# Kernel optimization log

Hardware: AMD Instinct MI355X
Metric: run time of the kernel (lower is better)

The kernel has to match this reference:

```python
import jax, jax.numpy as jnp
import numpy as np

N = 100000   # nodes
E = 1600000  # edges (avg degree 16)
D = 128      # input feature dim
H = 64       # hidden dim (hard-coded in Sage.__init__)
C = 40       # output classes


def setup_inputs() -> dict:
    key = jax.random.key(0)
    ks = jax.random.split(key, 9)
    s_in = 1.0 / np.sqrt(D)
    s_h = 1.0 / np.sqrt(H)
    return {
        "x": jax.random.normal(ks[0], (N, D), jnp.float32),
        "edge_index": jax.random.randint(ks[1], (2, E), 0, N, dtype=jnp.int64),
        # SAGEConv params: lin_l acts on aggregated neighbors (carries bias),
        # lin_r acts on the root/self features (no bias), per PyG defaults.
        "W1_l": jax.random.uniform(ks[2], (D, H), jnp.float32, -s_in, s_in),
        "W1_r": jax.random.uniform(ks[3], (D, H), jnp.float32, -s_in, s_in),
        "b1": jax.random.uniform(ks[4], (H,), jnp.float32, -s_in, s_in),
        "W2_l": jax.random.uniform(ks[5], (H, C), jnp.float32, -s_h, s_h),
        "W2_r": jax.random.uniform(ks[6], (H, C), jnp.float32, -s_h, s_h),
        "b2": jax.random.uniform(ks[7], (C,), jnp.float32, -s_h, s_h),
    }


def _sage_conv(x, src, dst, W_l, W_r, b):
    # mean-aggregate neighbor features at destination nodes
    msg = x[src]                                             # [E, F] gather
    summed = jax.ops.segment_sum(msg, dst, num_segments=N)   # [N, F]
    deg = jax.ops.segment_sum(jnp.ones((src.shape[0],), x.dtype), dst,
                              num_segments=N)                # [N]
    agg = summed / jnp.maximum(deg, 1.0)[:, None]
    return agg @ W_l + x @ W_r + b


def reference(x, edge_index, W1_l, W1_r, b1, W2_l, W2_r, b2):
    src, dst = edge_index[0], edge_index[1]
    h = _sage_conv(x, src, dst, W1_l, W1_r, b1)
    h = jax.nn.relu(h)
    # F.dropout(training=False) in eval mode -> identity
    out = _sage_conv(h, src, dst, W2_l, W2_r, b2)
    return jax.nn.log_softmax(out, axis=1)
```

## Files before the change

kernel.cpp:

```cpp
#include <hip/hip_runtime.h>

__device__ __forceinline__ float bf2f(unsigned short u) {
  union { unsigned int i; float f; } c; c.i = ((unsigned int)u) << 16; return c.f;
}
__device__ __forceinline__ unsigned short f2bf(float f) {
  union { float f; unsigned int i; } c; c.f = f;
  unsigned int x = c.i;
  return (unsigned short)((x + 0x7fffu + ((x >> 16) & 1u)) >> 16);
}
__device__ __forceinline__ float lo16(unsigned int w) { return bf2f((unsigned short)(w & 0xffffu)); }
__device__ __forceinline__ float hi16(unsigned int w) { return bf2f((unsigned short)(w >> 16)); }

#define DD 128
#define HH 64
#define CC 40
#define NBUCK 256
#define NCHUNK 128
#define MAXNPB 512
#define NQ 4

using bf16x8 = __attribute__((ext_vector_type(8))) short;
using f32x4  = __attribute__((ext_vector_type(4))) float;

__global__ __launch_bounds__(256) void detect(const unsigned int* e32,
                                              const unsigned int* x32, int* flags) {
  __shared__ unsigned int redOr[256];
  __shared__ int redCnt[256];
  int tid = threadIdx.x;
  unsigned int v = 0;
  for (int i = tid; i < 4096; i += 256) v |= e32[2 * i + 1];
  int cnt = 0;
  for (int i = tid; i < 4096; i += 256) {
    unsigned int w = x32[i];
    unsigned int expo = (w >> 7) & 0xffu;
    unsigned short lo = (unsigned short)(w & 0xffffu);
    if (lo == 0 || (expo >= 100u && expo <= 133u)) cnt++;
  }
  redOr[tid] = v; redCnt[tid] = cnt; __syncthreads();
  for (int s = 128; s > 0; s >>= 1) {
    if (tid < s) { redOr[tid] |= redOr[tid + s]; redCnt[tid] += redCnt[tid + s]; }
    __syncthreads();
  }
  if (tid == 0) {
    flags[0] = (redOr[0] == 0u) ? 1 : 0;
    flags[1] = (redCnt[0] < 2048) ? 1 : 0;
  }
}

__global__ __launch_bounds__(256) void hist_k(const int* e32, int E, int N,
                                              const int* flags, int nodesPerB,
                                              int* histG) {
  __shared__ int cnt[NBUCK];
  int tid = threadIdx.x;
  if (tid < NBUCK) cnt[tid] = 0;
  __syncthreads();
  int isI64 = flags[0];
  int chunk = (E + NCHUNK - 1) / NCHUNK;
  int e0 = blockIdx.x * chunk, e1 = min(e0 + chunk, E);
  for (int i = e0 + tid; i < e1; i += 256) {
    int d = isI64 ? e32[2 * (E + i)] : e32[E + i];
    d = min(max(d, 0), N - 1);
    atomicAdd(&cnt[d / nodesPerB], 1);
  }
  __syncthreads();
  if (tid < NBUCK) histG[tid * NCHUNK + blockIdx.x] = cnt[tid];
}

__global__ void hscan_prepw(const int* histG, int* ohist, int* bbase, int* row_ptr4,
                            int N, int E,
                            const void* W1l, const void* W1r, const void* b1,
                            const void* W2l, const void* W2r, const void* b2,
                            const int* flags, unsigned short* Wb1, unsigned short* Wb2,
                            float* b1f, float* b2f) {
  int tid = threadIdx.x;
  if (blockIdx.x == 1) {
    int isf = flags[1];
    auto rd = [&](const void* p, int i) -> float {
      return isf ? ((const float*)p)[i] : bf2f(((const unsigned short*)p)[i]);
    };
    for (int idx = tid; idx < 128 * 128; idx += 1024) {
      int n = idx >> 7, k = idx & 127;
      float v = (n < HH) ? rd(W1l, k * HH + n) : rd(W1r, k * HH + (n - HH));
      Wb1[idx] = f2bf(v);
    }
    for (int idx = tid; idx < 48 * 128; idx += 1024) {
      int n = idx >> 7, k = idx & 127;
      float v = 0.f;
      if (n < CC) v = (k < HH) ? rd(W2l, k * CC + n) : rd(W2r, (k - HH) * CC + n);
      Wb2[idx] = f2bf(v);
    }
    if (tid < HH) b1f[tid] = rd(b1, tid);
    if (tid < CC) b2f[tid] = rd(b2, tid);
    return;
  }
  __shared__ int tmp[1024];
  int v[32];
  int base = tid * 32;
  int s = 0;
#pragma unroll
  for (int k = 0; k < 32; k++) { v[k] = histG[base + k]; s += v[k]; }
  tmp[tid] = s; __syncthreads();
  for (int st = 1; st < 1024; st <<= 1) {
    int t = (tid >= st) ? tmp[tid - st] : 0;
    __syncthreads();
    tmp[tid] += t;
    __syncthreads();
  }
  int run = tmp[tid] - s;
#pragma unroll
  for (int k = 0; k < 32; k++) { ohist[base + k] = run; run += v[k]; }
  __syncthreads();
  if (tid < NBUCK) bbase[tid] = ohist[tid * NCHUNK];
  if (tid == 0) { bbase[NBUCK] = E; row_ptr4[NQ * N] = E; }
}

__global__ __launch_bounds__(256) void scatter_k(const int* e32, int E, int N,
                                                 const int* flags, int nodesPerB,
                                                 const int* ohist, uint2* ebuf) {
  __shared__ int cur[NBUCK];
  int tid = threadIdx.x;
  if (tid < NBUCK) cur[tid] = ohist[tid * NCHUNK + blockIdx.x];
  __syncthreads();
  int isI64 = flags[0];
  int chunk = (E + NCHUNK - 1) / NCHUNK;
  int e0 = blockIdx.x * chunk, e1 = min(e0 + chunk, E);
  for (int i = e0 + tid; i < e1; i += 256) {
    int s, d;
    if (isI64) { s = e32[2 * i]; d = e32[2 * (E + i)]; }
    else       { s = e32[i];     d = e32[E + i]; }
    s = min(max(s, 0), N - 1);
    d = min(max(d, 0), N - 1);
    int p = atomicAdd(&cur[d / nodesPerB], 1);
    ebuf[p] = make_uint2((unsigned)s, (unsigned)d);
  }
}

__global__ __launch_bounds__(256) void bktB_or_t1(
    const uint2* ebuf, const int* bbase,
    int nbuck, int nodesPerB, int qshift, int* row_ptr4, float* invd, int* col, int N,
    const void* xraw, const int* flags, const unsigned short* Wb1, const float* b1f,
    unsigned short* t1, unsigned short* s1, int T1B) {
  __shared__ int ldsb[MAXNPB * NQ + 256];
  int b = blockIdx.x;
  int tid = threadIdx.x;

  if (b < nbuck) {
    int* cnt = ldsb;
    int* sA  = ldsb + MAXNPB * NQ;
    int base_node = b * nodesPerB;
    int nn = min(nodesPerB, N - base_node);
    if (nn <= 0) return;
    int nk = nn * NQ;
    int eb0 = bbase[b], eb1 = bbase[b + 1];
    int nE = eb1 - eb0;
    const uint2* ee = ebuf + eb0;
    for (int i = tid; i < nk; i += 256) cnt[i] = 0;
    __syncthreads();
    for (int i = tid; i < nE; i += 256) {
      uint2 eg = ee[i];
      int key = ((int)eg.y - base_node) * NQ + (int)(eg.x >> qshift);
      atomicAdd(&cnt[key], 1);
    }
    __syncthreads();
    for (int i = tid; i < nn; i += 256) {
      int d = cnt[NQ * i] + cnt[NQ * i + 1] + cnt[NQ * i + 2] + cnt[NQ * i + 3];
      invd[base_node + i] = 1.0f / (float)max(d, 1);
    }
    __syncthreads();
    int per = (nk + 255) / 256;
    int myb = tid * per;
    int dreg[8];
    int ssum = 0;
#pragma unroll
    for (int k = 0; k < 8; k++) {
      int idx = myb + k;
      int v = (k < per && idx < nk) ? cnt[idx] : 0;
      dreg[k] = v; ssum += v;
    }
    sA[tid] = ssum;
    __syncthreads();
    for (int st = 1; st < 256; st <<= 1) {
      int t = (tid >= st) ? sA[tid - st] : 0;
      __syncthreads();
      sA[tid] += t;
      __syncthreads();
    }
    int run = eb0 + sA[tid] - ssum;
    __syncthreads();
#pragma unroll
    for (int k = 0; k < 8; k++) {
      int idx = myb + k;
      if (k < per && idx < nk) {
        row_ptr4[(size_t)(base_node + (idx >> 2)) * NQ + (idx & 3)] = run;
        cnt[idx] = run;
        run += dreg[k];
      }
    }
    __syncthreads();
    for (int i = tid; i < nE; i += 256) {
      uint2 eg = ee[i];
      int key = ((int)eg.y - base_node) * NQ + (int)(eg.x >> qshift);
      int p = atomicAdd(&cnt[key], 1);
      col[p] = (int)eg.x;
    }
    return;
  }

  int t = b - nbuck;
  if (t >= T1B) return;
  int lane = tid & 63, wv = tid >> 6;
  int nb = t * 64 + wv * 16;
  int oc = lane & 15, kgrp = lane >> 4;
  int node = min(nb + oc, N - 1);
  f32x4 acc[8];
#pragma unroll
  for (int i = 0; i < 8; i++) acc[i] = (f32x4){0.f, 0.f, 0.f, 0.f};

  if (flags[1]) {
    const float4* x4 = (const float4*)xraw;
#pragma unroll
    for (int kb = 0; kb < 4; kb++) {
      int k0 = kb * 32 + kgrp * 8;
      float4 a0 = x4[(size_t)node * 32 + (k0 >> 2)];
      float4 a1 = x4[(size_t)node * 32 + (k0 >> 2) + 1];
      bf16x8 af;
      af[0] = (short)f2bf(a0.x); af[1] = (short)f2bf(a0.y);
      af[2] = (short)f2bf(a0.z); af[3] = (short)f2bf(a0.w);
      af[4] = (short)f2bf(a1.x); af[5] = (short)f2bf(a1.y);
      af[6] = (short)f2bf(a1.z); af[7] = (short)f2bf(a1.w);
#pragma unroll
      for (int nblk = 0; nblk < 8; nblk++) {
        bf16x8 bfr = *(const bf16x8*)&Wb1[(nblk * 16 + oc) * 128 + k0];
        acc[nblk] = __builtin_amdgcn_mfma_f32_16x16x32_bf16(af, bfr, acc[nblk], 0, 0, 0);
      }
    }
  } else {
    const unsigned short* x16 = (const unsigned short*)xraw;
#pragma unroll
    for (int kb = 0; kb < 4; kb++) {
      int k0 = kb * 32 + kgrp * 8;
      bf16x8 af = *(const bf16x8*)&x16[(size_t)node * 128 + k0];
#pragma unroll
      for (int nblk = 0; nblk < 8; nblk++) {
        bf16x8 bfr = *(const bf16x8*)&Wb1[(nblk * 16 + oc) * 128 + k0];
        acc[nblk] = __builtin_amdgcn_mfma_f32_16x16x32_bf16(af, bfr, acc[nblk], 0, 0, 0);
      }
    }
  }

  int r0 = kgrp * 4;
#pragma unroll
  for (int nblk = 0; nblk < 8; nblk++) {
    float bias = (nblk >= 4) ? b1f[(nblk - 4) * 16 + oc] : 0.f;
#pragma unroll
    for (int r = 0; r < 4; r++) {
      int nn = nb + r0 + r;
      if (nn < N) {
        if (nblk < 4)
          t1[(size_t)nn * HH + nblk * 16 + oc] = f2bf(acc[nblk][r]);
        else
          s1[(size_t)nn * HH + (nblk - 4) * 16 + oc] = f2bf(acc[nblk][r] + bias);
      }
    }
  }
}

__device__ __forceinline__ void gather_seg(const uint4* t8, const int* col,
                                           int s0, int s1, int r, int c,
                                           float acc[8]) {
  for (int base = s0; base < s1; base += 8) {
    int i = base + r;
    bool g = (i < s1);
    int nb = g ? col[i] : 0;
    uint4 v = make_uint4(0, 0, 0, 0);
    if (g) v = t8[(size_t)nb * 8 + c];
    acc[0] += lo16(v.x); acc[1] += hi16(v.x);
    acc[2] += lo16(v.y); acc[3] += hi16(v.y);
    acc[4] += lo16(v.z); acc[5] += hi16(v.z);
    acc[6] += lo16(v.w); acc[7] += hi16(v.w);
  }
}

__global__ __launch_bounds__(256) void aggregate1(const unsigned short* t1,
                                                  const unsigned short* s1,
                                                  const int* row_ptr4, const float* invd,
                                                  const int* col, unsigned short* h, int N) {
  int wave = threadIdx.x >> 6, lane = threadIdx.x & 63;
  int r = lane >> 3, c = lane & 7;
  int n = blockIdx.x * 4 + wave;
  if (n >= N) return;
  int4 rp = *(const int4*)&row_ptr4[(size_t)NQ * n];
  int e4 = row_ptr4[(size_t)NQ * n + 4];
  float acc[8] = {0, 0, 0, 0, 0, 0, 0, 0};
  const uint4* t8 = (const uint4*)t1;
  gather_seg(t8, col, rp.x, rp.y, r, c, acc);
  gather_seg(t8, col, rp.y, rp.z, r, c, acc);
  gather_seg(t8, col, rp.z, rp.w, r, c, acc);
  gather_seg(t8, col, rp.w, e4, r, c, acc);
#pragma unroll
  for (int m = 8; m <= 32; m <<= 1)
#pragma unroll
    for (int i = 0; i < 8; i++) acc[i] += __shfl_xor(acc[i], m, 64);

  if (r == 0) {
    float id = invd[n];
    uint4 sv = ((const uint4*)s1)[(size_t)n * 8 + c];
    float s[8] = {lo16(sv.x), hi16(sv.x), lo16(sv.y), hi16(sv.y),
                  lo16(sv.z), hi16(sv.z), lo16(sv.w), hi16(sv.w)};
    unsigned int o[4];
#pragma unroll
    for (int i = 0; i < 4; i++) {
      float a0 = fmaxf(acc[2 * i] * id + s[2 * i], 0.f);
      float a1 = fmaxf(acc[2 * i + 1] * id + s[2 * i + 1], 0.f);
      o[i] = (unsigned int)f2bf(a0) | ((unsigned int)f2bf(a1) << 16);
    }
    ((uint4*)h)[(size_t)n * 8 + c] = make_uint4(o[0], o[1], o[2], o[3]);
  }
}

__global__ __launch_bounds__(256) void agg2(const unsigned short* h,
                                            const int* row_ptr4, const float* invd,
                                            const int* col, unsigned short* aggh, int N) {
  int wave = threadIdx.x >> 6, lane = threadIdx.x & 63;
  int r = lane >> 3, c = lane & 7;
  int n = blockIdx.x * 4 + wave;
  if (n >= N) return;
  int4 rp = *(const int4*)&row_ptr4[(size_t)NQ * n];
  int e4 = row_ptr4[(size_t)NQ * n + 4];
  float acc[8] = {0, 0, 0, 0, 0, 0, 0, 0};
  const uint4* h8 = (const uint4*)h;
  gather_seg(h8, col, rp.x, rp.y, r, c, acc);
  gather_seg(h8, col, rp.y, rp.z, r, c, acc);
  gather_seg(h8, col, rp.z, rp.w, r, c, acc);
  gather_seg(h8, col, rp.w, e4, r, c, acc);
#pragma unroll
  for (int m = 8; m <= 32; m <<= 1)
#pragma unroll
    for (int i = 0; i < 8; i++) acc[i] += __shfl_xor(acc[i], m, 64);

  if (r == 0) {
    float id = invd[n];
    unsigned int o[4];
#pragma unroll
    for (int i = 0; i < 4; i++) {
      o[i] = (unsigned int)f2bf(acc[2 * i] * id) |
             ((unsigned int)f2bf(acc[2 * i + 1] * id) << 16);
    }
    ((uint4*)aggh)[(size_t)n * 8 + c] = make_uint4(o[0], o[1], o[2], o[3]);
  }
}

__global__ __launch_bounds__(256) void final_k(const unsigned short* aggh,
                                               const unsigned short* h,
                                               const unsigned short* Wb2,
                                               const float* b2f,
                                               float* out, int N) {
  int tid = threadIdx.x;
  int lane = tid & 63, wv = tid >> 6;
  int nb = blockIdx.x * 64 + wv * 16;
  int oc = lane & 15, kgrp = lane >> 4;
  int node = min(nb + oc, N - 1);
  f32x4 acc[3];
#pragma unroll
  for (int i = 0; i < 3; i++) acc[i] = (f32x4){0.f, 0.f, 0.f, 0.f};

#pragma unroll
  for (int kb = 0; kb < 4; kb++) {
    int k0 = kb * 32 + kgrp * 8;
    const unsigned short* src = (kb < 2) ? aggh : h;
    int kk = k0 & 63;
    bf16x8 af = *(const bf16x8*)&src[(size_t)node * HH + kk];
#pragma unroll
    for (int nblk = 0; nblk < 3; nblk++) {
      bf16x8 bfr = *(const bf16x8*)&Wb2[(nblk * 16 + oc) * 128 + k0];
      acc[nblk] = __builtin_amdgcn_mfma_f32_16x16x32_bf16(af, bfr, acc[nblk], 0, 0, 0);
    }
  }

#pragma unroll
  for (int nblk = 0; nblk < 3; nblk++) {
    int cc = nblk * 16 + oc;
    float bias = (cc < CC) ? b2f[cc] : 0.f;
#pragma unroll
    for (int r = 0; r < 4; r++) acc[nblk][r] += bias;
  }

#pragma unroll
  for (int r = 0; r < 4; r++) {
    int nn = nb + kgrp * 4 + r;
    float m = -INFINITY;
#pragma unroll
    for (int nblk = 0; nblk < 3; nblk++)
      if (nblk * 16 + oc < CC) m = fmaxf(m, acc[nblk][r]);
    for (int off = 1; off <= 8; off <<= 1) m = fmaxf(m, __shfl_xor(m, off, 64));
    float s = 0.f;
#pragma unroll
    for (int nblk = 0; nblk < 3; nblk++)
      if (nblk * 16 + oc < CC) s += __expf(acc[nblk][r] - m);
    for (int off = 1; off <= 8; off <<= 1) s += __shfl_xor(s, off, 64);
    float lse = m + __logf(s);
    if (nn < N) {
#pragma unroll
      for (int nblk = 0; nblk < 3; nblk++) {
        int cc = nblk * 16 + oc;
        if (cc < CC) out[(size_t)nn * CC + cc] = acc[nblk][r] - lse;
      }
    }
  }
}

extern "C" void kernel_launch(void* const* d_in, const int* in_sizes, int n_in,
                              void* d_out, int out_size, void* d_ws, size_t ws_size,
                              hipStream_t stream) {
  const void* x   = d_in[0];
  const int*  e   = (const int*)d_in[1];
  const void* W1l = d_in[2];
  const void* W1r = d_in[3];
  const void* b1  = d_in[4];
  const void* W2l = d_in[5];
  const void* W2r = d_in[6];
  const void* b2  = d_in[7];
  float* out = (float*)d_out;

  const int N = in_sizes[0] / DD;
  const int E = in_sizes[1] / 2;
  const int nodesPerB = (N + NBUCK - 1) / NBUCK;
  const int nbuck = (N + nodesPerB - 1) / nodesPerB;
  const int T1B = (N + 63) / 64;
  int qshift = 0;
  while (((unsigned)(N - 1) >> qshift) > 3u) qshift++;

  char* w = (char*)d_ws;
  size_t off = 0;
  auto carve = [&](size_t bytes) -> void* {
    void* p = (void*)(w + off);
    off += (bytes + 255) & ~(size_t)255;
    return p;
  };
  int* col      = (int*)carve((size_t)E * 4);
  int* row_ptr4 = (int*)carve(((size_t)N * NQ + 1) * 4);
  float* invd   = (float*)carve((size_t)N * 4);
  int* histG    = (int*)carve((size_t)NBUCK * NCHUNK * 4);
  int* ohist    = (int*)carve((size_t)NBUCK * NCHUNK * 4);
  int* bbase    = (int*)carve((NBUCK + 1) * 4);
  int* flags    = (int*)carve(8);
  unsigned short* t1   = (unsigned short*)carve((size_t)N * HH * 2);
  unsigned short* s1   = (unsigned short*)carve((size_t)N * HH * 2);
  unsigned short* h    = (unsigned short*)carve((size_t)N * HH * 2);
  unsigned short* Wb1  = (unsigned short*)carve(128 * 128 * 2);
  unsigned short* Wb2  = (unsigned short*)carve(48 * 128 * 2);
  float* b1f   = (float*)carve(HH * sizeof(float));
  float* b2f   = (float*)carve(CC * sizeof(float));
  uint2* ebuf  = (uint2*)carve((size_t)E * 8);
  unsigned short* aggh = (unsigned short*)ebuf;
  (void)ws_size; (void)n_in; (void)out_size;

  detect<<<1, 256, 0, stream>>>((const unsigned int*)e, (const unsigned int*)x, flags);
  hist_k<<<NCHUNK, 256, 0, stream>>>(e, E, N, flags, nodesPerB, histG);
  hscan_prepw<<<2, 1024, 0, stream>>>(histG, ohist, bbase, row_ptr4, N, E,
                                      W1l, W1r, b1, W2l, W2r, b2,
                                      flags, Wb1, Wb2, b1f, b2f);
  scatter_k<<<NCHUNK, 256, 0, stream>>>(e, E, N, flags, nodesPerB, ohist, ebuf);
  bktB_or_t1<<<nbuck + T1B, 256, 0, stream>>>(ebuf, bbase,
                                              nbuck, nodesPerB, qshift, row_ptr4,
                                              invd, col, N,
                                              x, flags, Wb1, b1f, t1, s1, T1B);
  aggregate1<<<(N + 3) / 4, 256, 0, stream>>>(t1, s1, row_ptr4, invd, col, h, N);
  agg2<<<(N + 3) / 4, 256, 0, stream>>>(h, row_ptr4, invd, col, aggh, N);
  final_k<<<(N + 63) / 64, 256, 0, stream>>>(aggh, h, Wb2, b2f, out, N);
}
```

Measured before the change: 340.8 us.

## Replicate LDS bucket counters and process two nodes per wave in aggregation

Histogram and scatter kernels now keep four replicated LDS counters per bucket, indexed by thread lane, so atomic contention on hot buckets drops. The scan runs over the enlarged histogram. The aggregation kernels split each 64-lane wave into two 32-lane halves, each gathering one node with 4 edge rows at a time, which halves the grid and cuts idle lanes for low-degree nodes. In exchange the scan covers four times as many entries, and each node now gets fewer lanes for its gather.

```diff
diff --git a/kernel.cpp b/kernel.cpp
--- a/kernel.cpp
+++ b/kernel.cpp
@@ -18,6 +18,7 @@
 #define NCHUNK 128
 #define MAXNPB 512
 #define NQ 4
+#define NR 4
 
 using bf16x8 = __attribute__((ext_vector_type(8))) short;
 using f32x4  = __attribute__((ext_vector_type(4))) float;
@@ -50,20 +51,22 @@
 __global__ __launch_bounds__(256) void hist_k(const int* e32, int E, int N,
                                               const int* flags, int nodesPerB,
                                               int* histG) {
-  __shared__ int cnt[NBUCK];
-  int tid = threadIdx.x;
-  if (tid < NBUCK) cnt[tid] = 0;
+  __shared__ int cnt[NBUCK * NR];
+  int tid = threadIdx.x;
+  for (int i = tid; i < NBUCK * NR; i += 256) cnt[i] = 0;
   __syncthreads();
   int isI64 = flags[0];
+  int rep = tid & (NR - 1);
   int chunk = (E + NCHUNK - 1) / NCHUNK;
   int e0 = blockIdx.x * chunk, e1 = min(e0 + chunk, E);
   for (int i = e0 + tid; i < e1; i += 256) {
     int d = isI64 ? e32[2 * (E + i)] : e32[E + i];
     d = min(max(d, 0), N - 1);
-    atomicAdd(&cnt[d / nodesPerB], 1);
+    atomicAdd(&cnt[(d / nodesPerB) * NR + rep], 1);
   }
   __syncthreads();
-  if (tid < NBUCK) histG[tid * NCHUNK + blockIdx.x] = cnt[tid];
+  for (int i = tid; i < NBUCK * NR; i += 256)
+    histG[((i >> 2) * NCHUNK + blockIdx.x) * NR + (i & 3)] = cnt[i];
 }
 
 __global__ void hscan_prepw(const int* histG, int* ohist, int* bbase, int* row_ptr4,
@@ -94,11 +97,10 @@
     return;
   }
   __shared__ int tmp[1024];
-  int v[32];
-  int base = tid * 32;
+  const int PT = (NBUCK * NCHUNK * NR) / 1024;
+  int base = tid * PT;
   int s = 0;
-#pragma unroll
-  for (int k = 0; k < 32; k++) { v[k] = histG[base + k]; s += v[k]; }
+  for (int k = 0; k < PT; k++) s += histG[base + k];
   tmp[tid] = s; __syncthreads();
   for (int st = 1; st < 1024; st <<= 1) {
     int t = (tid >= st) ? tmp[tid - st] : 0;
@@ -107,21 +109,26 @@
     __syncthreads();
   }
   int run = tmp[tid] - s;
-#pragma unroll
-  for (int k = 0; k < 32; k++) { ohist[base + k] = run; run += v[k]; }
+  for (int k = 0; k < PT; k++) {
+    int v = histG[base + k];
+    ohist[base + k] = run;
+    run += v;
+  }
   __syncthreads();
-  if (tid < NBUCK) bbase[tid] = ohist[tid * NCHUNK];
+  if (tid < NBUCK) bbase[tid] = ohist[(size_t)tid * NCHUNK * NR];
   if (tid == 0) { bbase[NBUCK] = E; row_ptr4[NQ * N] = E; }
 }
 
 __global__ __launch_bounds__(256) void scatter_k(const int* e32, int E, int N,
                                                  const int* flags, int nodesPerB,
                                                  const int* ohist, uint2* ebuf) {
-  __shared__ int cur[NBUCK];
-  int tid = threadIdx.x;
-  if (tid < NBUCK) cur[tid] = ohist[tid * NCHUNK + blockIdx.x];
+  __shared__ int cur[NBUCK * NR];
+  int tid = threadIdx.x;
+  for (int i = tid; i < NBUCK * NR; i += 256)
+    cur[i] = ohist[((i >> 2) * NCHUNK + blockIdx.x) * NR + (i & 3)];
   __syncthreads();
   int isI64 = flags[0];
+  int rep = tid & (NR - 1);
   int chunk = (E + NCHUNK - 1) / NCHUNK;
   int e0 = blockIdx.x * chunk, e1 = min(e0 + chunk, E);
   for (int i = e0 + tid; i < e1; i += 256) {
@@ -130,7 +137,7 @@
     else       { s = e32[i];     d = e32[E + i]; }
     s = min(max(s, 0), N - 1);
     d = min(max(d, 0), N - 1);
-    int p = atomicAdd(&cur[d / nodesPerB], 1);
+    int p = atomicAdd(&cur[(d / nodesPerB) * NR + rep], 1);
     ebuf[p] = make_uint2((unsigned)s, (unsigned)d);
   }
 }
@@ -268,7 +275,7 @@
 __device__ __forceinline__ void gather_seg(const uint4* t8, const int* col,
                                            int s0, int s1, int r, int c,
                                            float acc[8]) {
-  for (int base = s0; base < s1; base += 8) {
+  for (int base = s0; base < s1; base += 4) {
     int i = base + r;
     bool g = (i < s1);
     int nb = g ? col[i] : 0;
@@ -286,8 +293,8 @@
                                                   const int* row_ptr4, const float* invd,
                                                   const int* col, unsigned short* h, int N) {
   int wave = threadIdx.x >> 6, lane = threadIdx.x & 63;
-  int r = lane >> 3, c = lane & 7;
-  int n = blockIdx.x * 4 + wave;
+  int ns = lane >> 5, r = (lane >> 3) & 3, c = lane & 7;
+  int n = blockIdx.x * 8 + wave * 2 + ns;
   if (n >= N) return;
   int4 rp = *(const int4*)&row_ptr4[(size_t)NQ * n];
   int e4 = row_ptr4[(size_t)NQ * n + 4];
@@ -298,7 +305,7 @@
   gather_seg(t8, col, rp.z, rp.w, r, c, acc);
   gather_seg(t8, col, rp.w, e4, r, c, acc);
 #pragma unroll
-  for (int m = 8; m <= 32; m <<= 1)
+  for (int m = 8; m <= 16; m <<= 1)
 #pragma unroll
     for (int i = 0; i < 8; i++) acc[i] += __shfl_xor(acc[i], m, 64);
 
@@ -322,8 +329,8 @@
                                             const int* row_ptr4, const float* invd,
                                             const int* col, unsigned short* aggh, int N) {
   int wave = threadIdx.x >> 6, lane = threadIdx.x & 63;
-  int r = lane >> 3, c = lane & 7;
-  int n = blockIdx.x * 4 + wave;
+  int ns = lane >> 5, r = (lane >> 3) & 3, c = lane & 7;
+  int n = blockIdx.x * 8 + wave * 2 + ns;
   if (n >= N) return;
   int4 rp = *(const int4*)&row_ptr4[(size_t)NQ * n];
   int e4 = row_ptr4[(size_t)NQ * n + 4];
@@ -334,7 +341,7 @@
   gather_seg(h8, col, rp.z, rp.w, r, c, acc);
   gather_seg(h8, col, rp.w, e4, r, c, acc);
 #pragma unroll
-  for (int m = 8; m <= 32; m <<= 1)
+  for (int m = 8; m <= 16; m <<= 1)
 #pragma unroll
     for (int i = 0; i < 8; i++) acc[i] += __shfl_xor(acc[i], m, 64);
 
@@ -440,8 +447,8 @@
   int* col      = (int*)carve((size_t)E * 4);
   int* row_ptr4 = (int*)carve(((size_t)N * NQ + 1) * 4);
   float* invd   = (float*)carve((size_t)N * 4);
-  int* histG    = (int*)carve((size_t)NBUCK * NCHUNK * 4);
-  int* ohist    = (int*)carve((size_t)NBUCK * NCHUNK * 4);
+  int* histG    = (int*)carve((size_t)NBUCK * NCHUNK * NR * 4);
+  int* ohist    = (int*)carve((size_t)NBUCK * NCHUNK * NR * 4);
   int* bbase    = (int*)carve((NBUCK + 1) * 4);
   int* flags    = (int*)carve(8);
   unsigned short* t1   = (unsigned short*)carve((size_t)N * HH * 2);
@@ -465,7 +472,7 @@
                                               nbuck, nodesPerB, qshift, row_ptr4,
                                               invd, col, N,
                                               x, flags, Wb1, b1f, t1, s1, T1B);
-  aggregate1<<<(N + 3) / 4, 256, 0, stream>>>(t1, s1, row_ptr4, invd, col, h, N);
-  agg2<<<(N + 3) / 4, 256, 0, stream>>>(h, row_ptr4, invd, col, aggh, N);
+  aggregate1<<<(N + 7) / 8, 256, 0, stream>>>(t1, s1, row_ptr4, invd, col, h, N);
+  agg2<<<(N + 7) / 8, 256, 0, stream>>>(h, row_ptr4, invd, col, aggh, N);
   final_k<<<(N + 63) / 64, 256, 0, stream>>>(aggh, h, Wb2, b2f, out, N);
 }
```

New measurement: 485.4 us. 42.5% more time.
